# Kernel tuning notes

Measured on AMD Instinct MI355X. Metric: run time of the kernel, lower is better.

The kernel has to match this reference:

```python
import jax, jax.numpy as jnp
import numpy as np
from jax import lax

N = 4096        # num graph nodes
T = 8           # timesteps (LSTM batch dim in original, batch_first=False)
IN_DIM = 64
H = 128         # hidden_dim
OUT_DIM = 1
E_RAND = 65536  # random edges; self-loops appended -> E = 69632


def setup_inputs() -> dict:
    key = jax.random.key(0)
    ks = jax.random.split(key, 18)
    s = 0.05
    f = lambda k, shp: (jax.random.normal(k, shp, jnp.float32) * s)
    src = jnp.concatenate([jax.random.randint(ks[15], (E_RAND,), 0, N), jnp.arange(N)]).astype(jnp.int32)
    dst = jnp.concatenate([jax.random.randint(ks[16], (E_RAND,), 0, N), jnp.arange(N)]).astype(jnp.int32)
    return {
        "input": jax.random.normal(ks[0], (N, T, IN_DIM), jnp.float32),
        "hidden": f(ks[1], (1, T, H)),
        "cell": f(ks[2], (1, T, H)),
        "pre_w": f(ks[3], (IN_DIM, H)),
        "pre_b": f(ks[4], (H,)),
        "w_ih": f(ks[5], (4 * H, H)),
        "w_hh": f(ks[6], (4 * H, H)),
        "b_ih": f(ks[7], (4 * H,)),
        "b_hh": f(ks[8], (4 * H,)),
        "gat_wsrc": f(ks[9], (H, H)),
        "gat_wdst": f(ks[10], (H, H)),
        "gat_attn": f(ks[11], (H,)),
        "gat_b": f(ks[12], (H,)),
        "out_w": f(ks[13], (H, OUT_DIM)),
        "out_b": f(ks[14], (OUT_DIM,)),
        "edge_src": src,
        "edge_dst": dst,
    }


def reference(input, hidden, cell, pre_w, pre_b, w_ih, w_hh, b_ih, b_hh,
              gat_wsrc, gat_wdst, gat_attn, gat_b, out_w, out_b,
              edge_src, edge_dst):
    n_nodes = input.shape[0]
    x = input @ pre_w + pre_b                         # (N, T, H)
    b = b_ih + b_hh

    # LSTM over node dimension (seq = nodes); the T per-timestep runs of the
    # original Python loop are independent (init states come from the given
    # hidden/cell), so we batch them along T.
    def step(carry, x_n):                             # x_n: (T, H)
        h, c = carry
        g = x_n @ w_ih.T + h @ w_hh.T + b             # (T, 4H), torch gate order i,f,g,o
        i_g, f_g, g_g, o_g = jnp.split(g, 4, axis=-1)
        c = jax.nn.sigmoid(f_g) * c + jax.nn.sigmoid(i_g) * jnp.tanh(g_g)
        h = jax.nn.sigmoid(o_g) * jnp.tanh(c)
        return (h, c), h

    (hT, cT), outs = lax.scan(step, (hidden[0], cell[0]), x)   # outs: (N, T, H)

    # GATv2Conv (DGL semantics, num_heads=1, share_weights=False)
    fs = outs @ gat_wsrc                              # (N, T, H)
    fd = outs @ gat_wdst
    e = jax.nn.leaky_relu(fs[edge_src] + fd[edge_dst], 0.2)    # (E, T, H)
    logits = e @ gat_attn                             # (E, T)
    # edge softmax per destination node (numerically stable)
    m = lax.stop_gradient(jax.ops.segment_max(logits, edge_dst, num_segments=n_nodes))
    a = jnp.exp(logits - m[edge_dst])
    denom = jax.ops.segment_sum(a, edge_dst, num_segments=n_nodes)
    alpha = a / denom[edge_dst]                       # (E, T)
    agg = jax.ops.segment_sum(alpha[..., None] * fs[edge_src], edge_dst, num_segments=n_nodes)
    rst = agg + gat_b                                 # (N, T, H)

    # dropout is identity in eval mode
    y = rst @ out_w + out_b                           # (N, T, OUT_DIM)
    return (y, hT[None], cT[None])
```

## Files before the change

kernel.cpp:

```cpp
#include <hip/hip_runtime.h>
#include <hip/hip_bf16.h>

#define N_NODES 4096
#define T_STEPS 8
#define INDIM   64
#define HDIM    128
#define G4      512
#define NROWS   (N_NODES * T_STEPS)
#define LOG2E   1.4426950408889634f

typedef __hip_bfloat16 bf16;
typedef __attribute__((ext_vector_type(8))) short bf16x8;
typedef __attribute__((ext_vector_type(4))) float f32x4;
typedef __attribute__((ext_vector_type(8))) int   i32x8;

__device__ __forceinline__ float asfloat_u(unsigned int u) {
    union { unsigned int i; float f; } v; v.i = u; return v.f;
}
__device__ __forceinline__ float fexp2(float x) {
    float r; asm("v_exp_f32 %0, %1" : "=v"(r) : "v"(x)); return r;
}

#define P_O0 32768
#define P_O1 (P_O0 + 512)
#define P_O2 (P_O1 + 16384)
#define P_O3 (P_O2 + 16384)
#define P_O4 (P_O3 + 128)
#define P_O5 (P_O4 + 1)
#define P_O6 (P_O5 + 65536)
#define P_O7 (P_O6 + 128)
__global__ void prep_kernel(const float* __restrict__ pre_w, const float* __restrict__ pre_b,
                            const float* __restrict__ w_ih, const float* __restrict__ b_ih,
                            const float* __restrict__ b_hh, const float* __restrict__ w_hh,
                            const float* __restrict__ wsrc, const float* __restrict__ wdst,
                            const float* __restrict__ out_w, const float* __restrict__ out_b,
                            const float* __restrict__ gat_b, const float* __restrict__ attn,
                            float* __restrict__ Wc, float* __restrict__ bc,
                            float* __restrict__ wsT, float* __restrict__ wdT,
                            float* __restrict__ wso, float* __restrict__ cy,
                            unsigned char* __restrict__ whh8, float* __restrict__ attn2) {
    int id = blockIdx.x * 256 + threadIdx.x;
    if (id < P_O0) {
        int g = id >> 6, i = id & 63;
        float s = 0.f;
        for (int k = 0; k < HDIM; k++) s += pre_w[i * HDIM + k] * w_ih[g * HDIM + k];
        int gate = g >> 7;
        Wc[id] = s * ((gate == 2) ? -2.f * LOG2E : -LOG2E);
    } else if (id < P_O1) {
        int g = id - P_O0;
        float s = b_ih[g] + b_hh[g];
        for (int k = 0; k < HDIM; k++) s += pre_b[k] * w_ih[g * HDIM + k];
        int gate = g >> 7;
        bc[g] = s * ((gate == 2) ? -2.f * LOG2E : -LOG2E);
    } else if (id < P_O2) {
        int c = id - P_O1;
        int co = c >> 7, k = c & 127;
        wsT[c] = wsrc[k * HDIM + co];
    } else if (id < P_O3) {
        int c = id - P_O2;
        int co = c >> 7, k = c & 127;
        wdT[c] = wdst[k * HDIM + co];
    } else if (id < P_O4) {
        int hi = id - P_O3;
        float s = 0.f;
        for (int ho = 0; ho < HDIM; ho++) s += wsrc[hi * HDIM + ho] * out_w[ho];
        wso[hi] = s;
    } else if (id == P_O4) {
        float s = out_b[0];
        for (int h = 0; h < HDIM; h++) s += gat_b[h] * out_w[h];
        cy[0] = s;
    } else if (id < P_O6) {
        int c = id - P_O5;
        int gate = c >> 14;
        float v = w_hh[c] * ((gate == 2) ? -2.f * LOG2E : -LOG2E);
        int pk = __builtin_amdgcn_cvt_pk_fp8_f32(v, v, 0, false);
        whh8[c] = (unsigned char)(pk & 0xff);
    } else if (id < P_O7) {
        int c = id - P_O6;
        attn2[c] = attn[c] * LOG2E;
    }
}

__global__ __launch_bounds__(512) void xw_kernel(const float* __restrict__ input,
                                                 const float* __restrict__ Wc,
                                                 const float* __restrict__ bc,
                                                 bf16* __restrict__ xw) {
    __shared__ __align__(16) float in_lds[16 * INDIM];
    int tid = threadIdx.x;
    int rowbase = blockIdx.x * 16;
    in_lds[tid]       = input[(size_t)rowbase * INDIM + tid];
    in_lds[tid + 512] = input[(size_t)rowbase * INDIM + tid + 512];
    __syncthreads();
    int g = tid;
    int gate = g >> 7, hh = g & 127;
    float4 w[16];
    const float4* wr = reinterpret_cast<const float4*>(Wc + g * INDIM);
#pragma unroll
    for (int u = 0; u < 16; u++) w[u] = wr[u];
    float b = bc[g];
    for (int r = 0; r < 16; r++) {
        const float4* hv = reinterpret_cast<const float4*>(in_lds + r * INDIM);
        float a0 = b, a1 = 0.f, a2 = 0.f, a3 = 0.f;
#pragma unroll
        for (int u = 0; u < 16; u++) {
            float4 h4 = hv[u]; float4 wv = w[u];
            a0 = fmaf(h4.x, wv.x, a0); a1 = fmaf(h4.y, wv.y, a1);
            a2 = fmaf(h4.z, wv.z, a2); a3 = fmaf(h4.w, wv.w, a3);
        }
        xw[(size_t)(rowbase + r) * G4 + hh * 4 + gate] = __float2bfloat16((a0 + a1) + (a2 + a3));
    }
}

__global__ __launch_bounds__(512, 1) void lstm_kernel(const bf16* __restrict__ xw,
                                                      const unsigned char* __restrict__ whh8,
                                                      const float* __restrict__ hidden0,
                                                      const float* __restrict__ cell0,
                                                      float* __restrict__ outs,
                                                      float* __restrict__ dout,
                                                      const int* __restrict__ esrc,
                                                      const int* __restrict__ edst,
                                                      int nE,
                                                      int* __restrict__ rowptr,
                                                      int* __restrict__ ssrc) {
    __shared__ __align__(16) char hbuf0[4 * 144];
    __shared__ __align__(16) char hbuf1[4 * 144];
    __shared__ int cnt[N_NODES];
    __shared__ int part[512];
    const int tid  = threadIdx.x;

    if (blockIdx.x == 2) {
        for (int i = tid; i < N_NODES; i += 512) cnt[i] = 0;
        __syncthreads();
        for (int i = tid; i < nE; i += 512) atomicAdd(&cnt[edst[i]], 1);
        __syncthreads();
        int base = tid * 8, loc[8], s = 0;
#pragma unroll
        for (int j = 0; j < 8; j++) { loc[j] = s; s += cnt[base + j]; }
        part[tid] = s;
        __syncthreads();
        for (int off = 1; off < 512; off <<= 1) {
            int v = (tid >= off) ? part[tid - off] : 0;
            __syncthreads();
            part[tid] += v;
            __syncthreads();
        }
        int pre = part[tid] - s;
#pragma unroll
        for (int j = 0; j < 8; j++) rowptr[base + j] = pre + loc[j];
        if (tid == 511) rowptr[N_NODES] = nE;
        __syncthreads();
#pragma unroll
        for (int j = 0; j < 8; j++) cnt[base + j] = pre + loc[j];
        __syncthreads();
        for (int i = tid; i < nE; i += 512) {
            int d = edst[i];
            int pos = atomicAdd(&cnt[d], 1);
            ssrc[pos] = esrc[i];
        }
        return;
    }

    const int w    = tid >> 6;
    const int lane = tid & 63;
    const int kg   = lane >> 4;
    const int lr   = lane & 15;
    const int q    = lr & 3;
    const int d    = lr >> 2;
    const int qg   = blockIdx.x * 4 + q;
    const int hb   = 16 * w + kg * 4 + d;

    i32x8 afr[4];
#pragma unroll
    for (int G = 0; G < 4; G++) {
        const unsigned char* rowp = whh8 + (size_t)(G * 128 + 16 * w + lr) * HDIM + kg * 32;
        afr[G] = *reinterpret_cast<const i32x8*>(rowp);
    }

    const int roff = q * 144 + kg * 32;
    const int woff = q * 144 + hb;
    const int sc   = 0x7f7f7f7f;

    float cv = cell0[qg * HDIM + hb];
    float hv = hidden0[qg * HDIM + hb];
    {
        int pk = __builtin_amdgcn_cvt_pk_fp8_f32(hv, hv, 0, false);
        *reinterpret_cast<unsigned char*>(hbuf0 + woff) = (unsigned char)(pk & 0xff);
    }

    const uint2* xq = reinterpret_cast<const uint2*>(xw) + qg * 128 + hb;
    float* outp = outs + qg * HDIM + hb;

    uint2 xb[8];
#pragma unroll
    for (int i = 0; i < 8; i++) xb[i] = xq[i * 1024];
    __syncthreads();

#define STEPX(NIDX, RB, WB, XQ)                                                      \
    do {                                                                             \
        i32x8 bfr = *reinterpret_cast<const i32x8*>(RB + roff);                      \
        f32x4 z = {0.f, 0.f, 0.f, 0.f};                                              \
        f32x4 acc0 = __builtin_amdgcn_mfma_scale_f32_16x16x128_f8f6f4(               \
            afr[0], bfr, z, 0, 0, 0, sc, 0, sc);                                     \
        f32x4 acc1 = __builtin_amdgcn_mfma_scale_f32_16x16x128_f8f6f4(               \
            afr[1], bfr, z, 0, 0, 0, sc, 0, sc);                                     \
        f32x4 acc2 = __builtin_amdgcn_mfma_scale_f32_16x16x128_f8f6f4(               \
            afr[2], bfr, z, 0, 0, 0, sc, 0, sc);                                     \
        f32x4 acc3 = __builtin_amdgcn_mfma_scale_f32_16x16x128_f8f6f4(               \
            afr[3], bfr, z, 0, 0, 0, sc, 0, sc);                                     \
        float s0 = (d & 2) ? ((d & 1) ? acc0[3] : acc0[2])                           \
                           : ((d & 1) ? acc0[1] : acc0[0]);                          \
        float s1 = (d & 2) ? ((d & 1) ? acc1[3] : acc1[2])                           \
                           : ((d & 1) ? acc1[1] : acc1[0]);                          \
        float s2 = (d & 2) ? ((d & 1) ? acc2[3] : acc2[2])                           \
                           : ((d & 1) ? acc2[1] : acc2[0]);                          \
        float s3 = (d & 2) ? ((d & 1) ? acc3[3] : acc3[2])                           \
                           : ((d & 1) ? acc3[1] : acc3[0]);                          \
        float gi = s0 + asfloat_u((XQ).x << 16);                                     \
        float gf = s1 + asfloat_u((XQ).x & 0xffff0000u);                             \
        float gg = s2 + asfloat_u((XQ).y << 16);                                     \
        float go = s3 + asfloat_u((XQ).y & 0xffff0000u);                             \
        float A = fexp2(gi), C = fexp2(gf), B = fexp2(gg);                           \
        float p = 1.f + A, r = 1.f + B, s = 1.f + C;                                 \
        float pr = p * r;                                                            \
        float num = fmaf(cv, pr, (2.f - r) * s);                                     \
        cv = num * __builtin_amdgcn_rcpf(pr * s);                                    \
        float O = fexp2(go), F = fexp2(cv * (-2.f * LOG2E));                         \
        float po = 1.f + O, rf = 1.f + F;                                            \
        hv = (2.f - rf) * __builtin_amdgcn_rcpf(po * rf);                            \
        int pk = __builtin_amdgcn_cvt_pk_fp8_f32(hv, hv, 0, false);                  \
        *reinterpret_cast<unsigned char*>(WB + woff) = (unsigned char)(pk & 0xff);   \
        outp[(NIDX) * 1024] = hv;                                                    \
        asm volatile("s_waitcnt lgkmcnt(0)" ::: "memory");                           \
        __builtin_amdgcn_s_barrier();                                                \
        __builtin_amdgcn_sched_barrier(0);                                           \
    } while (0)

    for (int n = 0; n < N_NODES; n += 8) {
#pragma unroll
        for (int i = 0; i < 8; i++) {
            if (i & 1) STEPX(n + i, hbuf1, hbuf0, xb[i]);
            else       STEPX(n + i, hbuf0, hbuf1, xb[i]);
            xb[i] = xq[(n + i + 8) * 1024];
        }
    }
#undef STEPX

    dout[NROWS + qg * HDIM + hb] = hv;
    dout[NROWS + T_STEPS * HDIM + qg * HDIM + hb] = cv;
}

__global__ __launch_bounds__(256) void fsfd_kernel(const float* __restrict__ outs,
                                                   const float* __restrict__ wsT,
                                                   const float* __restrict__ wdT,
                                                   const float* __restrict__ wso,
                                                   bf16* __restrict__ fs,
                                                   bf16* __restrict__ fd,
                                                   float* __restrict__ fso) {
    __shared__ __align__(16) float rows[32 * HDIM];
    int tid = threadIdx.x;
    size_t base = (size_t)blockIdx.x * 32 * HDIM;
#pragma unroll
    for (int j = 0; j < 16; j++) rows[tid + j * 256] = outs[base + tid + j * 256];
    __syncthreads();
    int c = tid;
    const float4* wT = reinterpret_cast<const float4*>(
        (c < HDIM) ? (wsT + c * HDIM) : (wdT + (c - HDIM) * HDIM));
    float4 w[32];
#pragma unroll
    for (int u = 0; u < 32; u++) w[u] = wT[u];
    bf16* dst = (c < HDIM) ? (fs + base + c) : (fd + base + (c - HDIM));
    for (int r = 0; r < 32; r++) {
        const float4* hv = reinterpret_cast<const float4*>(rows + r * HDIM);
        float a0 = 0.f, a1 = 0.f, a2 = 0.f, a3 = 0.f;
#pragma unroll
        for (int u = 0; u < 32; u++) {
            float4 h4 = hv[u]; float4 wv = w[u];
            a0 = fmaf(h4.x, wv.x, a0); a1 = fmaf(h4.y, wv.y, a1);
            a2 = fmaf(h4.z, wv.z, a2); a3 = fmaf(h4.w, wv.w, a3);
        }
        dst[(size_t)r * HDIM] = __float2bfloat16((a0 + a1) + (a2 + a3));
    }
    if (tid < 32) {
        const float* rp = rows + tid * HDIM;
        float s = 0.f;
        for (int k = 0; k < HDIM; k++) {
            int kk = (k + tid) & 127;
            s += rp[kk] * wso[kk];
        }
        fso[blockIdx.x * 32 + tid] = s;
    }
}

__global__ __launch_bounds__(256) void edge_csr_kernel(const int* __restrict__ ssrc,
                                                       const int* __restrict__ rowptr,
                                                       const bf16* __restrict__ fs,
                                                       const bf16* __restrict__ fd,
                                                       const float* __restrict__ attn2,
                                                       const float* __restrict__ fso,
                                                       const float* __restrict__ cy,
                                                       float* __restrict__ dout) {
    int dn = blockIdx.x * 4 + (threadIdx.x >> 6);
    int l  = threadIdx.x & 63;
    float a0 = attn2[2 * l], a1 = attn2[2 * l + 1];
    const unsigned int* fdp = reinterpret_cast<const unsigned int*>(fd) + (size_t)dn * 512 + l;
    unsigned int fdw[8];
#pragma unroll
    for (int t = 0; t < 8; t++) fdw[t] = fdp[t * 64];
    float den[8], num[8];
#pragma unroll
    for (int t = 0; t < 8; t++) { den[t] = 0.f; num[t] = 0.f; }
    int e0 = rowptr[dn], e1 = rowptr[dn + 1];
    for (int e = e0; e < e1; e++) {
        int s = ssrc[e];
        const unsigned int* fsp = reinterpret_cast<const unsigned int*>(fs) + (size_t)s * 512 + l;
        float4 fsoA = *reinterpret_cast<const float4*>(fso + s * 8);
        float4 fsoB = *reinterpret_cast<const float4*>(fso + s * 8 + 4);
        float fsov[8] = {fsoA.x, fsoA.y, fsoA.z, fsoA.w, fsoB.x, fsoB.y, fsoB.z, fsoB.w};
#pragma unroll
        for (int t = 0; t < 8; t++) {
            unsigned int uf = fsp[t * 64];
            float x1 = asfloat_u(uf << 16) + asfloat_u(fdw[t] << 16);
            float x2 = asfloat_u(uf & 0xffff0000u) + asfloat_u(fdw[t] & 0xffff0000u);
            x1 = fmaxf(x1, 0.f) + 0.2f * fminf(x1, 0.f);
            x2 = fmaxf(x2, 0.f) + 0.2f * fminf(x2, 0.f);
            float v = x1 * a0 + x2 * a1;
#pragma unroll
            for (int m = 32; m >= 1; m >>= 1) v += __shfl_xor(v, m, 64);
            float a = fexp2(v);
            den[t] += a;
            num[t] = fmaf(a, fsov[t], num[t]);
        }
    }
    if (l == 0) {
        float cyv = cy[0];
        float4 y0, y1;
        y0.x = num[0] * __builtin_amdgcn_rcpf(den[0]) + cyv;
        y0.y = num[1] * __builtin_amdgcn_rcpf(den[1]) + cyv;
        y0.z = num[2] * __builtin_amdgcn_rcpf(den[2]) + cyv;
        y0.w = num[3] * __builtin_amdgcn_rcpf(den[3]) + cyv;
        y1.x = num[4] * __builtin_amdgcn_rcpf(den[4]) + cyv;
        y1.y = num[5] * __builtin_amdgcn_rcpf(den[5]) + cyv;
        y1.z = num[6] * __builtin_amdgcn_rcpf(den[6]) + cyv;
        y1.w = num[7] * __builtin_amdgcn_rcpf(den[7]) + cyv;
        *reinterpret_cast<float4*>(dout + dn * 8)     = y0;
        *reinterpret_cast<float4*>(dout + dn * 8 + 4) = y1;
    }
}

extern "C" void kernel_launch(void* const* d_in, const int* in_sizes, int n_in,
                              void* d_out, int out_size, void* d_ws, size_t ws_size,
                              hipStream_t stream) {
    const float* input  = (const float*)d_in[0];
    const float* hidden = (const float*)d_in[1];
    const float* cell   = (const float*)d_in[2];
    const float* pre_w  = (const float*)d_in[3];
    const float* pre_b  = (const float*)d_in[4];
    const float* w_ih   = (const float*)d_in[5];
    const float* w_hh   = (const float*)d_in[6];
    const float* b_ih   = (const float*)d_in[7];
    const float* b_hh   = (const float*)d_in[8];
    const float* wsrc   = (const float*)d_in[9];
    const float* wdst   = (const float*)d_in[10];
    const float* attn   = (const float*)d_in[11];
    const float* gatb   = (const float*)d_in[12];
    const float* outw   = (const float*)d_in[13];
    const float* outb   = (const float*)d_in[14];
    const int*   esrc   = (const int*)d_in[15];
    const int*   edst   = (const int*)d_in[16];
    int nE = in_sizes[15];
    float* dout = (float*)d_out;
    char* ws = (char*)d_ws;

    const size_t o_xw    = 0;
    const size_t o_outs  = 33554432;
    const size_t o_fs    = 50331648;
    const size_t o_fd    = 58720256;
    const size_t o_fso   = 67108864;
    const size_t o_rowptr= 67272704;
    const size_t o_ssrc  = 67289344;
    const size_t o_wc    = 67502080;
    const size_t o_bc    = 67633152;
    const size_t o_wsT   = 67635200;
    const size_t o_wdT   = 67700736;
    const size_t o_wso   = 67766272;
    const size_t o_cy    = 67766784;
    const size_t o_attn2 = 67767040;
    const size_t o_whh8  = o_fs;

    bf16*  xw    = (bf16*)(ws + o_xw);
    float* outs  = (float*)(ws + o_outs);
    bf16*  fs    = (bf16*)(ws + o_fs);
    bf16*  fd    = (bf16*)(ws + o_fd);
    float* fso   = (float*)(ws + o_fso);
    int*   rowptr= (int*)(ws + o_rowptr);
    int*   ssrc  = (int*)(ws + o_ssrc);
    float* Wc    = (float*)(ws + o_wc);
    float* bc    = (float*)(ws + o_bc);
    float* wsT   = (float*)(ws + o_wsT);
    float* wdT   = (float*)(ws + o_wdT);
    float* wso   = (float*)(ws + o_wso);
    float* cy    = (float*)(ws + o_cy);
    float* attn2 = (float*)(ws + o_attn2);
    unsigned char* whh8 = (unsigned char*)(ws + o_whh8);

    prep_kernel<<<516, 256, 0, stream>>>(pre_w, pre_b, w_ih, b_ih, b_hh, w_hh, wsrc, wdst,
                                         outw, outb, gatb, attn,
                                         Wc, bc, wsT, wdT, wso, cy, whh8, attn2);
    xw_kernel<<<2048, 512, 0, stream>>>(input, Wc, bc, xw);
    lstm_kernel<<<3, 512, 0, stream>>>(xw, whh8, hidden, cell, outs, dout,
                                       esrc, edst, nE, rowptr, ssrc);
    fsfd_kernel<<<1024, 256, 0, stream>>>(outs, wsT, wdT, wso, fs, fd, fso);
    edge_csr_kernel<<<N_NODES / 4, 256, 0, stream>>>(ssrc, rowptr, fs, fd, attn2, fso, cy, dout);
}
```

Measured before the change: 1.660 ms.

## Split LSTM recurrence across four 256-thread blocks with two timesteps each

Repartitions the sequential LSTM scan from two 512-thread blocks (4 timestep columns each) into four 256-thread blocks (2 timestep columns each), with each wave now covering 32 hidden units via two MFMA tiles per gate. Each block's per-step barrier then spans 4 waves instead of 8, which shortens the synchronisation on the serial critical path. The cost is twice as many MFMAs per wave per step, half of each tile's output columns wasted, and more register pressure from eight weight fragments. The CSR-building block moves to index 4 and uses 256 threads, with a 16-element-per-thread scan.

Result: no change. 1.651 ms (median of 2 runs) (-0.5%).

```diff
diff --git a/kernel.cpp b/kernel.cpp
--- a/kernel.cpp
+++ b/kernel.cpp
@@ -111,7 +111,7 @@
     }
 }
 
-__global__ __launch_bounds__(512, 1) void lstm_kernel(const bf16* __restrict__ xw,
+__global__ __launch_bounds__(256, 1) void lstm_kernel(const bf16* __restrict__ xw,
                                                       const unsigned char* __restrict__ whh8,
                                                       const float* __restrict__ hidden0,
                                                       const float* __restrict__ cell0,
@@ -122,23 +122,23 @@
                                                       int nE,
                                                       int* __restrict__ rowptr,
                                                       int* __restrict__ ssrc) {
-    __shared__ __align__(16) char hbuf0[4 * 144];
-    __shared__ __align__(16) char hbuf1[4 * 144];
+    __shared__ __align__(16) char hbuf0[2 * 144];
+    __shared__ __align__(16) char hbuf1[2 * 144];
     __shared__ int cnt[N_NODES];
-    __shared__ int part[512];
+    __shared__ int part[256];
     const int tid  = threadIdx.x;
 
-    if (blockIdx.x == 2) {
-        for (int i = tid; i < N_NODES; i += 512) cnt[i] = 0;
+    if (blockIdx.x == 4) {
+        for (int i = tid; i < N_NODES; i += 256) cnt[i] = 0;
         __syncthreads();
-        for (int i = tid; i < nE; i += 512) atomicAdd(&cnt[edst[i]], 1);
+        for (int i = tid; i < nE; i += 256) atomicAdd(&cnt[edst[i]], 1);
         __syncthreads();
-        int base = tid * 8, loc[8], s = 0;
-#pragma unroll
-        for (int j = 0; j < 8; j++) { loc[j] = s; s += cnt[base + j]; }
+        int base = tid * 16, loc[16], s = 0;
+#pragma unroll
+        for (int j = 0; j < 16; j++) { loc[j] = s; s += cnt[base + j]; }
         part[tid] = s;
         __syncthreads();
-        for (int off = 1; off < 512; off <<= 1) {
+        for (int off = 1; off < 256; off <<= 1) {
             int v = (tid >= off) ? part[tid - off] : 0;
             __syncthreads();
             part[tid] += v;
@@ -146,13 +146,13 @@
         }
         int pre = part[tid] - s;
 #pragma unroll
-        for (int j = 0; j < 8; j++) rowptr[base + j] = pre + loc[j];
-        if (tid == 511) rowptr[N_NODES] = nE;
+        for (int j = 0; j < 16; j++) rowptr[base + j] = pre + loc[j];
+        if (tid == 255) rowptr[N_NODES] = nE;
         __syncthreads();
 #pragma unroll
-        for (int j = 0; j < 8; j++) cnt[base + j] = pre + loc[j];
+        for (int j = 0; j < 16; j++) cnt[base + j] = pre + loc[j];
         __syncthreads();
-        for (int i = tid; i < nE; i += 512) {
+        for (int i = tid; i < nE; i += 256) {
             int d = edst[i];
             int pos = atomicAdd(&cnt[d], 1);
             ssrc[pos] = esrc[i];
@@ -164,17 +164,21 @@
     const int lane = tid & 63;
     const int kg   = lane >> 4;
     const int lr   = lane & 15;
-    const int q    = lr & 3;
-    const int d    = lr >> 2;
-    const int qg   = blockIdx.x * 4 + q;
-    const int hb   = 16 * w + kg * 4 + d;
-
-    i32x8 afr[4];
-#pragma unroll
-    for (int G = 0; G < 4; G++) {
-        const unsigned char* rowp = whh8 + (size_t)(G * 128 + 16 * w + lr) * HDIM + kg * 32;
-        afr[G] = *reinterpret_cast<const i32x8*>(rowp);
-    }
+    const int q    = lr & 1;
+    const int d    = (lr >> 1) & 3;
+    const int b    = lr >> 3;
+    const int qg   = blockIdx.x * 2 + q;
+    const int hb   = 32 * w + 16 * b + kg * 4 + d;
+
+    i32x8 afr[4][2];
+#pragma unroll
+    for (int G = 0; G < 4; G++)
+#pragma unroll
+        for (int bb = 0; bb < 2; bb++) {
+            const unsigned char* rowp =
+                whh8 + (size_t)(G * 128 + 32 * w + 16 * bb + lr) * HDIM + kg * 32;
+            afr[G][bb] = *reinterpret_cast<const i32x8*>(rowp);
+        }
 
     const int roff = q * 144 + kg * 32;
     const int woff = q * 144 + hb;
@@ -195,30 +199,35 @@
     for (int i = 0; i < 8; i++) xb[i] = xq[i * 1024];
     __syncthreads();
 
+#define SEL(M) ((d & 2) ? ((d & 1) ? (M)[3] : (M)[2]) : ((d & 1) ? (M)[1] : (M)[0]))
 #define STEPX(NIDX, RB, WB, XQ)                                                      \
     do {                                                                             \
         i32x8 bfr = *reinterpret_cast<const i32x8*>(RB + roff);                      \
         f32x4 z = {0.f, 0.f, 0.f, 0.f};                                              \
-        f32x4 acc0 = __builtin_amdgcn_mfma_scale_f32_16x16x128_f8f6f4(               \
-            afr[0], bfr, z, 0, 0, 0, sc, 0, sc);                                     \
-        f32x4 acc1 = __builtin_amdgcn_mfma_scale_f32_16x16x128_f8f6f4(               \
-            afr[1], bfr, z, 0, 0, 0, sc, 0, sc);                                     \
-        f32x4 acc2 = __builtin_amdgcn_mfma_scale_f32_16x16x128_f8f6f4(               \
-            afr[2], bfr, z, 0, 0, 0, sc, 0, sc);                                     \
-        f32x4 acc3 = __builtin_amdgcn_mfma_scale_f32_16x16x128_f8f6f4(               \
-            afr[3], bfr, z, 0, 0, 0, sc, 0, sc);                                     \
-        float s0 = (d & 2) ? ((d & 1) ? acc0[3] : acc0[2])                           \
-                           : ((d & 1) ? acc0[1] : acc0[0]);                          \
-        float s1 = (d & 2) ? ((d & 1) ? acc1[3] : acc1[2])                           \
-                           : ((d & 1) ? acc1[1] : acc1[0]);                          \
-        float s2 = (d & 2) ? ((d & 1) ? acc2[3] : acc2[2])                           \
-                           : ((d & 1) ? acc2[1] : acc2[0]);                          \
-        float s3 = (d & 2) ? ((d & 1) ? acc3[3] : acc3[2])                           \
-                           : ((d & 1) ? acc3[1] : acc3[0]);                          \
-        float gi = s0 + asfloat_u((XQ).x << 16);                                     \
-        float gf = s1 + asfloat_u((XQ).x & 0xffff0000u);                             \
-        float gg = s2 + asfloat_u((XQ).y << 16);                                     \
-        float go = s3 + asfloat_u((XQ).y & 0xffff0000u);                             \
+        f32x4 a00 = __builtin_amdgcn_mfma_scale_f32_16x16x128_f8f6f4(                \
+            afr[0][0], bfr, z, 0, 0, 0, sc, 0, sc);                                  \
+        f32x4 a01 = __builtin_amdgcn_mfma_scale_f32_16x16x128_f8f6f4(                \
+            afr[0][1], bfr, z, 0, 0, 0, sc, 0, sc);                                  \
+        f32x4 a10 = __builtin_amdgcn_mfma_scale_f32_16x16x128_f8f6f4(                \
+            afr[1][0], bfr, z, 0, 0, 0, sc, 0, sc);                                  \
+        f32x4 a11 = __builtin_amdgcn_mfma_scale_f32_16x16x128_f8f6f4(                \
+            afr[1][1], bfr, z, 0, 0, 0, sc, 0, sc);                                  \
+        f32x4 a20 = __builtin_amdgcn_mfma_scale_f32_16x16x128_f8f6f4(                \
+            afr[2][0], bfr, z, 0, 0, 0, sc, 0, sc);                                  \
+        f32x4 a21 = __builtin_amdgcn_mfma_scale_f32_16x16x128_f8f6f4(                \
+            afr[2][1], bfr, z, 0, 0, 0, sc, 0, sc);                                  \
+        f32x4 a30 = __builtin_amdgcn_mfma_scale_f32_16x16x128_f8f6f4(                \
+            afr[3][0], bfr, z, 0, 0, 0, sc, 0, sc);                                  \
+        f32x4 a31 = __builtin_amdgcn_mfma_scale_f32_16x16x128_f8f6f4(                \
+            afr[3][1], bfr, z, 0, 0, 0, sc, 0, sc);                                  \
+        f32x4 m0 = b ? a01 : a00;                                                    \
+        f32x4 m1 = b ? a11 : a10;                                                    \
+        f32x4 m2 = b ? a21 : a20;                                                    \
+        f32x4 m3 = b ? a31 : a30;                                                    \
+        float gi = SEL(m0) + asfloat_u((XQ).x << 16);                                \
+        float gf = SEL(m1) + asfloat_u((XQ).x & 0xffff0000u);                        \
+        float gg = SEL(m2) + asfloat_u((XQ).y << 16);                                \
+        float go = SEL(m3) + asfloat_u((XQ).y & 0xffff0000u);                        \
         float A = fexp2(gi), C = fexp2(gf), B = fexp2(gg);                           \
         float p = 1.f + A, r = 1.f + B, s = 1.f + C;                                 \
         float pr = p * r;                                                            \
@@ -244,6 +253,7 @@
         }
     }
 #undef STEPX
+#undef SEL
 
     dout[NROWS + qg * HDIM + hb] = hv;
     dout[NROWS + T_STEPS * HDIM + qg * HDIM + hb] = cv;
@@ -407,7 +417,7 @@
                                          outw, outb, gatb, attn,
                                          Wc, bc, wsT, wdT, wso, cy, whh8, attn2);
     xw_kernel<<<2048, 512, 0, stream>>>(input, Wc, bc, xw);
-    lstm_kernel<<<3, 512, 0, stream>>>(xw, whh8, hidden, cell, outs, dout,
+    lstm_kernel<<<5, 256, 0, stream>>>(xw, whh8, hidden, cell, outs, dout,
                                        esrc, edst, nE, rowptr, ssrc);
     fsfd_kernel<<<1024, 256, 0, stream>>>(outs, wsT, wdT, wso, fs, fd, fso);
     edge_csr_kernel<<<N_NODES / 4, 256, 0, stream>>>(ssrc, rowptr, fs, fd, attn2, fso, cy, dout);
```
